# Kernel tuning notes

Hardware: AMD Instinct MI355X
Metric: run time of the kernel (lower is better)

## Reference

```python
import jax, jax.numpy as jnp
import numpy as np

EPS = 1e-5

def layer_norm(x, g, b):
    mu = jnp.mean(x, axis=-1, keepdims=True)
    var = jnp.var(x, axis=-1, keepdims=True)
    return (x - mu) * jax.lax.rsqrt(var + EPS) * g + b

def setup_inputs() -> dict:
    key = jax.random.key(0)
    ks = jax.random.split(key, 8)
    B, N, C, H = 4, 1024, 1024, 16
    Dh = C * 4
    std = 0.02
    return {
        "x": jax.random.normal(ks[0], (B, N, C), dtype=jnp.float32),
        "qkv_w": jax.random.normal(ks[1], (3 * C, C), dtype=jnp.float32) * std,
        "proj_w": jax.random.normal(ks[2], (C, C), dtype=jnp.float32) * std,
        "proj_b": jnp.zeros((C,), dtype=jnp.float32),
        "fc1_w": jax.random.normal(ks[3], (Dh, C), dtype=jnp.float32) * std,
        "fc1_b": jnp.zeros((Dh,), dtype=jnp.float32),
        "fc2_w": jax.random.normal(ks[4], (C, Dh), dtype=jnp.float32) * std,
        "fc2_b": jnp.zeros((C,), dtype=jnp.float32),
        "ln1_g": jnp.ones((C,), dtype=jnp.float32),
        "ln1_b": jnp.zeros((C,), dtype=jnp.float32),
        "ln2_g": jnp.ones((C,), dtype=jnp.float32),
        "ln2_b": jnp.zeros((C,), dtype=jnp.float32),
        "lnh_g": jnp.ones((Dh,), dtype=jnp.float32),
        "lnh_b": jnp.zeros((Dh,), dtype=jnp.float32),
    }

def reference(x, qkv_w, proj_w, proj_b, fc1_w, fc1_b, fc2_w, fc2_b,
              ln1_g, ln1_b, ln2_g, ln2_b, lnh_g, lnh_b):
    B, N, C = x.shape
    H = 16
    Dh = C // H
    scale = Dh ** (-0.5)

    # --- attention sublayer (pre-norm) ---
    h = layer_norm(x, ln1_g, ln1_b)
    qkv = (h @ qkv_w.T).reshape(B, N, 3, H, Dh).transpose(2, 0, 3, 1, 4)  # [3,B,H,N,Dh]
    q, k, v = qkv[0], qkv[1], qkv[2]
    attn = jnp.einsum('bhid,bhjd->bhij', q, k) * scale
    attn = jax.nn.softmax(attn, axis=-1)
    o = jnp.einsum('bhij,bhjd->bhid', attn, v)          # [B,H,N,Dh]
    o = o.transpose(0, 2, 1, 3).reshape(B, N, C)
    o = o @ proj_w.T + proj_b
    x = x + o

    # --- MLP sublayer (pre-norm, with LN on hidden per use_ln=True) ---
    h = layer_norm(x, ln2_g, ln2_b)
    u = jax.nn.gelu(h @ fc1_w.T + fc1_b, approximate=False)  # torch nn.GELU = erf form
    u = layer_norm(u, lnh_g, lnh_b)
    m = u @ fc2_w.T + fc2_b
    return x + m
```

## Files before the change

kernel.cpp:

```cpp
#include <hip/hip_runtime.h>
#include <hip/hip_bf16.h>
#include <math.h>


#define TOKENS 4096
#define CDIM   1024
#define HEADS  16
#define DHEAD  64
#define HID    4096

typedef __attribute__((ext_vector_type(4))) float  floatx4;
typedef __attribute__((ext_vector_type(8))) short  short8;

__device__ __forceinline__ void gl_lds16(const void* g, void* l)
{
    __builtin_amdgcn_global_load_lds(
        (const __attribute__((address_space(1))) unsigned int*)g,
        (__attribute__((address_space(3))) unsigned int*)l,
        16, 0, 0);
}

__global__ __launch_bounds__(256) void cvt_all(
    const float* __restrict__ s0, const float* __restrict__ s1,
    const float* __restrict__ s2, const float* __restrict__ s3,
    __hip_bfloat16* __restrict__ dst)
{
    long i = (long)blockIdx.x * 256 + threadIdx.x;
    const float* src;
    long base;
    if (i < 768l * 1024)       { src = s0; base = 0; }
    else if (i < 1792l * 1024) { src = s1; base = 768l * 1024; }
    else if (i < 2816l * 1024) { src = s2; base = 1792l * 1024; }
    else                       { src = s3; base = 2816l * 1024; }
    float4 v = ((const float4*)src)[i - base];
    __hip_bfloat16 t[4];
    t[0] = __float2bfloat16(v.x);
    t[1] = __float2bfloat16(v.y);
    t[2] = __float2bfloat16(v.z);
    t[3] = __float2bfloat16(v.w);
    *(uint2*)(dst + 4l * i) = *(uint2*)t;
}

__global__ __launch_bounds__(256) void ln_f32_kernel(
    const float* __restrict__ x, const float* __restrict__ g,
    const float* __restrict__ b, __hip_bfloat16* __restrict__ y, int C)
{
    int row = blockIdx.x;
    const float4* xr = (const float4*)(x + (long)row * C);
    uint2* yr = (uint2*)(y + (long)row * C);
    const int C4 = C >> 2;

    float s = 0.f, ss = 0.f;
    for (int i = threadIdx.x; i < C4; i += 256) {
        float4 v = xr[i];
        s  += v.x + v.y + v.z + v.w;
        ss += v.x * v.x + v.y * v.y + v.z * v.z + v.w * v.w;
    }
    #pragma unroll
    for (int d = 32; d; d >>= 1) {
        s  += __shfl_down(s, d);
        ss += __shfl_down(ss, d);
    }
    __shared__ float buf[4][2];
    int wid = threadIdx.x >> 6, lane = threadIdx.x & 63;
    if (lane == 0) { buf[wid][0] = s; buf[wid][1] = ss; }
    __syncthreads();
    if (threadIdx.x == 0) {
        s = buf[0][0] + buf[1][0] + buf[2][0] + buf[3][0];
        ss = buf[0][1] + buf[1][1] + buf[2][1] + buf[3][1];
        buf[0][0] = s; buf[0][1] = ss;
    }
    __syncthreads();
    s = buf[0][0]; ss = buf[0][1];

    float invC = 1.f / (float)C;
    float mu = s * invC;
    float var = ss * invC - mu * mu;
    float inv = rsqrtf(var + 1e-5f);
    const float4* gg = (const float4*)g;
    const float4* bb = (const float4*)b;
    for (int i = threadIdx.x; i < C4; i += 256) {
        float4 v = xr[i], gv = gg[i], bv = bb[i];
        __hip_bfloat16 t[4];
        t[0] = __float2bfloat16((v.x - mu) * inv * gv.x + bv.x);
        t[1] = __float2bfloat16((v.y - mu) * inv * gv.y + bv.y);
        t[2] = __float2bfloat16((v.z - mu) * inv * gv.z + bv.z);
        t[3] = __float2bfloat16((v.w - mu) * inv * gv.w + bv.w);
        yr[i] = *(uint2*)t;
    }
}

__global__ __launch_bounds__(256) void ln_bf16_kernel(
    const __hip_bfloat16* __restrict__ x, const float* __restrict__ g,
    const float* __restrict__ b, __hip_bfloat16* __restrict__ y, int C)
{
    int row = blockIdx.x;
    const uint4* xr = (const uint4*)(x + (long)row * C);
    uint4* yr = (uint4*)(y + (long)row * C);
    const int C8 = C >> 3;

    float s = 0.f, ss = 0.f;
    for (int i = threadIdx.x; i < C8; i += 256) {
        uint4 raw = xr[i];
        const __hip_bfloat16* p = (const __hip_bfloat16*)&raw;
        #pragma unroll
        for (int j = 0; j < 8; ++j) {
            float v = __bfloat162float(p[j]);
            s += v; ss += v * v;
        }
    }
    #pragma unroll
    for (int d = 32; d; d >>= 1) {
        s  += __shfl_down(s, d);
        ss += __shfl_down(ss, d);
    }
    __shared__ float buf[4][2];
    int wid = threadIdx.x >> 6, lane = threadIdx.x & 63;
    if (lane == 0) { buf[wid][0] = s; buf[wid][1] = ss; }
    __syncthreads();
    if (threadIdx.x == 0) {
        s = buf[0][0] + buf[1][0] + buf[2][0] + buf[3][0];
        ss = buf[0][1] + buf[1][1] + buf[2][1] + buf[3][1];
        buf[0][0] = s; buf[0][1] = ss;
    }
    __syncthreads();
    s = buf[0][0]; ss = buf[0][1];

    float invC = 1.f / (float)C;
    float mu = s * invC;
    float var = ss * invC - mu * mu;
    float inv = rsqrtf(var + 1e-5f);
    const float4* gg = (const float4*)g;
    const float4* bb = (const float4*)b;
    for (int i = threadIdx.x; i < C8; i += 256) {
        uint4 raw = xr[i];
        const __hip_bfloat16* p = (const __hip_bfloat16*)&raw;
        float4 g0 = gg[2 * i], g1 = gg[2 * i + 1];
        float4 b0 = bb[2 * i], b1 = bb[2 * i + 1];
        __hip_bfloat16 t[8];
        t[0] = __float2bfloat16((__bfloat162float(p[0]) - mu) * inv * g0.x + b0.x);
        t[1] = __float2bfloat16((__bfloat162float(p[1]) - mu) * inv * g0.y + b0.y);
        t[2] = __float2bfloat16((__bfloat162float(p[2]) - mu) * inv * g0.z + b0.z);
        t[3] = __float2bfloat16((__bfloat162float(p[3]) - mu) * inv * g0.w + b0.w);
        t[4] = __float2bfloat16((__bfloat162float(p[4]) - mu) * inv * g1.x + b1.x);
        t[5] = __float2bfloat16((__bfloat162float(p[5]) - mu) * inv * g1.y + b1.y);
        t[6] = __float2bfloat16((__bfloat162float(p[6]) - mu) * inv * g1.z + b1.z);
        t[7] = __float2bfloat16((__bfloat162float(p[7]) - mu) * inv * g1.w + b1.w);
        yr[i] = *(uint4*)t;
    }
}

__global__ __launch_bounds__(256, 2) void gemm_db(
    const __hip_bfloat16* __restrict__ A,
    const __hip_bfloat16* __restrict__ W,
    const float* __restrict__ bias, const float* __restrict__ residual,
    void* __restrict__ Cout, int M, int N, int K, int mode)
{
    __shared__ __align__(16) char Asl[2][16384];
    __shared__ __align__(16) char Bsl[2][16384];

    int tid = threadIdx.x;
    int wave = tid >> 6, lane = tid & 63;

    int mt, nt;
    {
        int gx = gridDim.x, gy = gridDim.y;
        int lin = blockIdx.y * gx + blockIdx.x;
        int chunk = gy >> 3;
        int xcd = lin & 7, q = lin >> 3;
        mt = xcd * chunk + (q % chunk);
        nt = q / chunk;
    }
    int bm = mt * 128, bn = nt * 128;
    int wm = wave & 1, wn = wave >> 1;
    int fm = lane & 15, quad = lane >> 4;
    const int r7 = fm & 7;

    const int nk = K / 64;

    const int rsub = lane >> 3;
    const int csub = (lane & 7) ^ rsub;
    const __hip_bfloat16* gA[4];
    const __hip_bfloat16* gB[4];
    int dseg[4];
    #pragma unroll
    for (int j = 0; j < 4; ++j) {
        int seg = wave * 4 + j;
        gA[j] = A + (long)(bm + seg * 8 + rsub) * K + csub * 8;
        gB[j] = W + (long)(bn + seg * 8 + rsub) * K + csub * 8;
        dseg[j] = seg * 1024;
    }

#define STAGE(b, kt) { \
    const long ko = (long)(kt) * 64; \
    _Pragma("unroll") \
    for (int j = 0; j < 4; ++j) { \
        gl_lds16(gA[j] + ko, Asl[b] + dseg[j]); \
        gl_lds16(gB[j] + ko, Bsl[b] + dseg[j]); \
    } }

    floatx4 acc[4][4] = {};

    STAGE(0, 0);
    __syncthreads();

    int cur = 0;
    for (int kt = 0; kt < nk; ++kt) {
        if (kt + 1 < nk) STAGE(cur ^ 1, kt + 1);

        const char* Ab = Asl[cur];
        const char* Bb = Bsl[cur];
        #pragma unroll
        for (int kh = 0; kh < 2; ++kh) {
            const int xsw = ((kh * 4 + quad) ^ r7) << 4;
            short8 bq[4];
            #pragma unroll
            for (int j = 0; j < 4; ++j)
                bq[j] = *(const short8*)(Bb + (wn * 64 + j * 16 + fm) * 128 + xsw);
            #pragma unroll
            for (int i = 0; i < 4; ++i) {
                short8 af = *(const short8*)(Ab + (wm * 64 + i * 16 + fm) * 128 + xsw);
                #pragma unroll
                for (int j = 0; j < 4; ++j)
                    acc[i][j] = __builtin_amdgcn_mfma_f32_16x16x32_bf16(
                        af, bq[j], acc[i][j], 0, 0, 0);
            }
        }
        __syncthreads();
        cur ^= 1;
    }
#undef STAGE

    int mbase = bm + wm * 64;
    int nbase = bn + wn * 64;
    if (mode == 2) {
        float* Cf = (float*)Cout;
        #pragma unroll
        for (int i = 0; i < 4; ++i) {
            #pragma unroll
            for (int j = 0; j < 4; ++j) {
                int ncol = nbase + j * 16 + fm;
                float bv = bias[ncol];
                #pragma unroll
                for (int r = 0; r < 4; ++r) {
                    int mrow = mbase + i * 16 + quad * 4 + r;
                    long idx = (long)mrow * N + ncol;
                    Cf[idx] = acc[i][j][r] + bv + residual[idx];
                }
            }
        }
    } else {
        __hip_bfloat16* Cb = (__hip_bfloat16*)Cout;
        #pragma unroll
        for (int i = 0; i < 4; ++i) {
            #pragma unroll
            for (int j = 0; j < 4; ++j) {
                int ncol = nbase + j * 16 + fm;
                #pragma unroll
                for (int r = 0; r < 4; ++r) {
                    int mrow = mbase + i * 16 + quad * 4 + r;
                    float v = acc[i][j][r];
                    if (bias) v += bias[ncol];
                    if (mode == 1) {
                        float z = v * (1.5957691216f + 0.0713548162f * v * v);
                        v = v / (1.f + __expf(-z));
                    }
                    Cb[(long)mrow * N + ncol] = __float2bfloat16(v);
                }
            }
        }
    }
}

__global__ __launch_bounds__(256) void attn_mfma(
    const __hip_bfloat16* __restrict__ qkv, __hip_bfloat16* __restrict__ o_out)
{
    __shared__ __align__(16) char Ks[2][64 * 144];
    __shared__ __align__(16) char Vt[2][64 * 144];
    __shared__ __align__(16) char Ps[4 * 16 * 144];

    const int C3 = 3 * CDIM;
    int lin = blockIdx.x;
    int xcd = lin & 7, q = lin >> 3;
    int bh = xcd * 8 + (q >> 4);
    int qt = q & 15;
    int b = bh >> 4, hh = bh & 15;
    int tid = threadIdx.x, wave = tid >> 6, lane = tid & 63;
    int l = lane & 15, quad = lane >> 4;

    const __hip_bfloat16* qrow =
        qkv + (long)(b * 1024 + qt * 64 + wave * 16 + l) * C3 + hh * DHEAD;
    short8 qf0 = *(const short8*)(qrow + quad * 8);
    short8 qf1 = *(const short8*)(qrow + 32 + quad * 8);

    char* Psw = Ps + wave * (16 * 144);

    int sc = tid & 7;
    int skl = tid >> 3;

    const __hip_bfloat16* Kbase = qkv + (long)(b * 1024) * C3 + CDIM + hh * DHEAD;
    const __hip_bfloat16* Vbase = qkv + (long)(b * 1024) * C3 + 2 * CDIM + hh * DHEAD;
    const int kpp = skl ^ (sc << 2);

    floatx4 facc[4] = {};
    float mrun = -1e30f, lrun = 0.f;

    uint4 kA0, kA1, vA0, vA1;
    uint4 kB0, kB1, vB0, vB1;

#define GKV(t, k0, k1, v0, v1) { \
    const __hip_bfloat16* Kg = Kbase + (long)((t) * 64) * C3; \
    const __hip_bfloat16* Vg = Vbase + (long)((t) * 64) * C3; \
    k0 = *(const uint4*)(Kg + (long)skl * C3 + sc * 8); \
    k1 = *(const uint4*)(Kg + (long)(skl + 32) * C3 + sc * 8); \
    v0 = *(const uint4*)(Vg + (long)(2 * skl) * C3 + sc * 8); \
    v1 = *(const uint4*)(Vg + (long)(2 * skl + 1) * C3 + sc * 8); }
#define WKV(bf, k0, k1, v0, v1) { \
    *(uint4*)(Ks[bf] + skl * 144 + sc * 16) = k0; \
    *(uint4*)(Ks[bf] + (skl + 32) * 144 + sc * 16) = k1; \
    const ushort* e0 = (const ushort*)&v0; \
    const ushort* e1 = (const ushort*)&v1; \
    _Pragma("unroll") \
    for (int j = 0; j < 8; ++j) { \
        unsigned dw = (unsigned)e0[j] | ((unsigned)e1[j] << 16); \
        *(unsigned*)(Vt[bf] + (sc * 8 + j) * 144 + kpp * 4) = dw; \
    } }

    auto compute = [&](int buf) {
        floatx4 st[4] = {};
        #pragma unroll
        for (int kb = 0; kb < 4; ++kb) {
            short8 k0 = *(const short8*)(Ks[buf] + (kb * 16 + l) * 144 + quad * 16);
            short8 k1 = *(const short8*)(Ks[buf] + (kb * 16 + l) * 144 + 64 + quad * 16);
            st[kb] = __builtin_amdgcn_mfma_f32_16x16x32_bf16(k0, qf0, st[kb], 0, 0, 0);
            st[kb] = __builtin_amdgcn_mfma_f32_16x16x32_bf16(k1, qf1, st[kb], 0, 0, 0);
        }
        float p[16];
        float tm = -1e30f;
        #pragma unroll
        for (int kb = 0; kb < 4; ++kb)
            #pragma unroll
            for (int r = 0; r < 4; ++r) {
                float s = st[kb][r] * 0.125f;
                p[kb * 4 + r] = s;
                tm = fmaxf(tm, s);
            }
        tm = fmaxf(tm, __shfl_xor(tm, 16));
        tm = fmaxf(tm, __shfl_xor(tm, 32));
        float mn = fmaxf(mrun, tm);
        float alpha = __expf(mrun - mn);
        float psum = 0.f;
        #pragma unroll
        for (int i = 0; i < 16; ++i) { p[i] = __expf(p[i] - mn); psum += p[i]; }
        psum += __shfl_xor(psum, 16);
        psum += __shfl_xor(psum, 32);
        lrun = lrun * alpha + psum;
        mrun = mn;

        #pragma unroll
        for (int kb = 0; kb < 4; ++kb) {
            __hip_bfloat16 t[4];
            #pragma unroll
            for (int r = 0; r < 4; ++r) t[r] = __float2bfloat16(p[kb * 4 + r]);
            *(uint2*)(Psw + l * 144 + kb * 32 + quad * 8) = *(const uint2*)t;
        }

        float a0 = __shfl(alpha, quad * 4 + 0);
        float a1 = __shfl(alpha, quad * 4 + 1);
        float a2 = __shfl(alpha, quad * 4 + 2);
        float a3 = __shfl(alpha, quad * 4 + 3);
        #pragma unroll
        for (int db = 0; db < 4; ++db) {
            facc[db][0] *= a0; facc[db][1] *= a1;
            facc[db][2] *= a2; facc[db][3] *= a3;
        }

        short8 pf0 = *(const short8*)(Psw + l * 144 + quad * 16);
        short8 pf1 = *(const short8*)(Psw + l * 144 + 64 + quad * 16);
        #pragma unroll
        for (int db = 0; db < 4; ++db) {
            int d = db * 16 + l;
            int o3 = (d >> 3) & 7;
            short8 v0 = *(const short8*)(Vt[buf] + d * 144 + ((quad ^ o3) << 4));
            short8 v1 = *(const short8*)(Vt[buf] + d * 144 + (((4 + quad) ^ o3) << 4));
            facc[db] = __builtin_amdgcn_mfma_f32_16x16x32_bf16(pf0, v0, facc[db], 0, 0, 0);
            facc[db] = __builtin_amdgcn_mfma_f32_16x16x32_bf16(pf1, v1, facc[db], 0, 0, 0);
        }
    };

    GKV(0, kA0, kA1, vA0, vA1);
    #pragma unroll 1
    for (int kt = 0; kt < 16; kt += 2) {
        WKV(0, kA0, kA1, vA0, vA1);
        __syncthreads();
        GKV(kt + 1, kB0, kB1, vB0, vB1);
        compute(0);
        WKV(1, kB0, kB1, vB0, vB1);
        __syncthreads();
        if (kt + 2 < 16) GKV(kt + 2, kA0, kA1, vA0, vA1);
        compute(1);
    }
#undef GKV
#undef WKV

    float il0 = 1.f / __shfl(lrun, quad * 4 + 0);
    float il1 = 1.f / __shfl(lrun, quad * 4 + 1);
    float il2 = 1.f / __shfl(lrun, quad * 4 + 2);
    float il3 = 1.f / __shfl(lrun, quad * 4 + 3);
    __hip_bfloat16* orow =
        o_out + (long)(b * 1024 + qt * 64 + wave * 16) * CDIM + hh * DHEAD;
    #pragma unroll
    for (int db = 0; db < 4; ++db) {
        int col = db * 16 + l;
        orow[(quad * 4 + 0) * CDIM + col] = __float2bfloat16(facc[db][0] * il0);
        orow[(quad * 4 + 1) * CDIM + col] = __float2bfloat16(facc[db][1] * il1);
        orow[(quad * 4 + 2) * CDIM + col] = __float2bfloat16(facc[db][2] * il2);
        orow[(quad * 4 + 3) * CDIM + col] = __float2bfloat16(facc[db][3] * il3);
    }
}

extern "C" void kernel_launch(void* const* d_in, const int* in_sizes, int n_in,
                              void* d_out, int out_size, void* d_ws, size_t ws_size,
                              hipStream_t stream)
{
    const float* x      = (const float*)d_in[0];
    const float* qkv_w  = (const float*)d_in[1];
    const float* proj_w = (const float*)d_in[2];
    const float* proj_b = (const float*)d_in[3];
    const float* fc1_w  = (const float*)d_in[4];
    const float* fc1_b  = (const float*)d_in[5];
    const float* fc2_w  = (const float*)d_in[6];
    const float* fc2_b  = (const float*)d_in[7];
    const float* ln1_g  = (const float*)d_in[8];
    const float* ln1_b  = (const float*)d_in[9];
    const float* ln2_g  = (const float*)d_in[10];
    const float* ln2_b  = (const float*)d_in[11];
    const float* lnh_g  = (const float*)d_in[12];
    const float* lnh_b  = (const float*)d_in[13];

    float* out = (float*)d_out;

    __hip_bfloat16* wsb     = (__hip_bfloat16*)d_ws;
    __hip_bfloat16* qkvw_bf = wsb;
    __hip_bfloat16* fc1w_bf = qkvw_bf + 3l * 1024 * 1024;
    __hip_bfloat16* fc2w_bf = fc1w_bf + 4l * 1024 * 1024;
    __hip_bfloat16* projw_bf= fc2w_bf + 4l * 1024 * 1024;
    __hip_bfloat16* h_bf    = projw_bf + 1l * 1024 * 1024;
    __hip_bfloat16* qkv_bf  = h_bf + 4l * 1024 * 1024;
    __hip_bfloat16* o_bf    = qkv_bf + 12l * 1024 * 1024;
    __hip_bfloat16* u_bf    = o_bf + 4l * 1024 * 1024;

    cvt_all<<<12288, 256, 0, stream>>>(qkv_w, fc1_w, fc2_w, proj_w, qkvw_bf);

    ln_f32_kernel<<<TOKENS, 256, 0, stream>>>(x, ln1_g, ln1_b, h_bf, CDIM);
    gemm_db<<<dim3(3072 / 128, TOKENS / 128), 256, 0, stream>>>(
        h_bf, qkvw_bf, nullptr, nullptr, qkv_bf, TOKENS, 3072, CDIM, 0);
    attn_mfma<<<1024, 256, 0, stream>>>(qkv_bf, o_bf);
    gemm_db<<<dim3(CDIM / 128, TOKENS / 128), 256, 0, stream>>>(
        o_bf, projw_bf, proj_b, x, out, TOKENS, CDIM, CDIM, 2);
    ln_f32_kernel<<<TOKENS, 256, 0, stream>>>(out, ln2_g, ln2_b, h_bf, CDIM);
    gemm_db<<<dim3(HID / 128, TOKENS / 128), 256, 0, stream>>>(
        h_bf, fc1w_bf, fc1_b, nullptr, u_bf, TOKENS, HID, CDIM, 1);
    ln_bf16_kernel<<<TOKENS, 256, 0, stream>>>(u_bf, lnh_g, lnh_b, u_bf, HID);
    gemm_db<<<dim3(CDIM / 128, TOKENS / 128), 256, 0, stream>>>(
        u_bf, fc2w_bf, fc2_b, out, out, TOKENS, CDIM, HID, 2);
}
```

Measured before the change: 386.7 us.

## Split GEMM into K=32 128x128 kernel and 64x64 tile kernel for N=1024 GEMMs

Replaces the single 128x128, K=64 double-buffered GEMM with two specialized kernels. For the wide QKV and FC1 GEMMs, a 128x128 tile with K-step 32 halves LDS usage, which allows 4 blocks per CU and uses a new swizzled layout packing two 64-row halves per LDS row. For the narrow proj and FC2 GEMMs (N=1024), a 64x64 tile kernel launches 4x more blocks to fill the GPU, but each block gets less data reuse and runs more k-iteration syncs.

```diff
diff --git a/kernel.cpp b/kernel.cpp
--- a/kernel.cpp
+++ b/kernel.cpp
@@ -150,14 +150,14 @@
     }
 }
 
-__global__ __launch_bounds__(256, 2) void gemm_db(
+__global__ __launch_bounds__(256, 4) void gemm32q(
     const __hip_bfloat16* __restrict__ A,
     const __hip_bfloat16* __restrict__ W,
-    const float* __restrict__ bias, const float* __restrict__ residual,
-    void* __restrict__ Cout, int M, int N, int K, int mode)
-{
-    __shared__ __align__(16) char Asl[2][16384];
-    __shared__ __align__(16) char Bsl[2][16384];
+    const float* __restrict__ bias,
+    __hip_bfloat16* __restrict__ Cout, int M, int N, int K, int mode)
+{
+    __shared__ __align__(16) char Asl[2][8192];
+    __shared__ __align__(16) char Bsl[2][8192];
 
     int tid = threadIdx.x;
     int wave = tid >> 6, lane = tid & 63;
@@ -174,32 +174,137 @@
     int bm = mt * 128, bn = nt * 128;
     int wm = wave & 1, wn = wave >> 1;
     int fm = lane & 15, quad = lane >> 4;
-    const int r7 = fm & 7;
+
+    const int nk = K / 32;
+
+    const int rsub  = lane >> 3;
+    const int cphys = lane & 7;
+    const int clog  = cphys ^ rsub;
+    const __hip_bfloat16* gA[2];
+    const __hip_bfloat16* gB[2];
+    int dseg[2];
+    #pragma unroll
+    for (int j = 0; j < 2; ++j) {
+        int seg = wave * 2 + j;
+        int ldsrow = seg * 8 + rsub;
+        int mrow = ldsrow + 64 * (clog >> 2);
+        int koff = (clog & 3) * 8;
+        gA[j] = A + (long)(bm + mrow) * K + koff;
+        gB[j] = W + (long)(bn + mrow) * K + koff;
+        dseg[j] = seg * 1024;
+    }
+
+#define STAGE(b, kt) { \
+    const long ko = (long)(kt) * 32; \
+    _Pragma("unroll") \
+    for (int j = 0; j < 2; ++j) { \
+        gl_lds16(gA[j] + ko, Asl[b] + dseg[j]); \
+        gl_lds16(gB[j] + ko, Bsl[b] + dseg[j]); \
+    } }
+
+    floatx4 acc[4][4] = {};
+
+    STAGE(0, 0);
+    __syncthreads();
+
+    const int xswA = (((wm * 4 + quad) ^ (fm & 7)) << 4);
+    const int xswB = (((wn * 4 + quad) ^ (fm & 7)) << 4);
+
+    int cur = 0;
+    for (int kt = 0; kt < nk; ++kt) {
+        if (kt + 1 < nk) STAGE(cur ^ 1, kt + 1);
+
+        const char* Ab = Asl[cur];
+        const char* Bb = Bsl[cur];
+        short8 bq[4];
+        #pragma unroll
+        for (int j = 0; j < 4; ++j)
+            bq[j] = *(const short8*)(Bb + (j * 16 + fm) * 128 + xswB);
+        #pragma unroll
+        for (int i = 0; i < 4; ++i) {
+            short8 af = *(const short8*)(Ab + (i * 16 + fm) * 128 + xswA);
+            #pragma unroll
+            for (int j = 0; j < 4; ++j)
+                acc[i][j] = __builtin_amdgcn_mfma_f32_16x16x32_bf16(
+                    af, bq[j], acc[i][j], 0, 0, 0);
+        }
+        __syncthreads();
+        cur ^= 1;
+    }
+#undef STAGE
+
+    int mbase = bm + wm * 64;
+    int nbase = bn + wn * 64;
+    #pragma unroll
+    for (int i = 0; i < 4; ++i) {
+        #pragma unroll
+        for (int j = 0; j < 4; ++j) {
+            int ncol = nbase + j * 16 + fm;
+            #pragma unroll
+            for (int r = 0; r < 4; ++r) {
+                int mrow = mbase + i * 16 + quad * 4 + r;
+                float v = acc[i][j][r];
+                if (bias) v += bias[ncol];
+                if (mode == 1) {
+                    float z = v * (1.5957691216f + 0.0713548162f * v * v);
+                    v = v / (1.f + __expf(-z));
+                }
+                Cout[(long)mrow * N + ncol] = __float2bfloat16(v);
+            }
+        }
+    }
+}
+
+__global__ __launch_bounds__(256, 4) void gemm64g(
+    const __hip_bfloat16* __restrict__ A,
+    const __hip_bfloat16* __restrict__ W,
+    const float* __restrict__ bias, const float* __restrict__ residual,
+    float* __restrict__ Cout, int M, int N, int K)
+{
+    __shared__ __align__(16) char Asl[2][8192];
+    __shared__ __align__(16) char Bsl[2][8192];
+
+    int tid = threadIdx.x;
+    int wave = tid >> 6, lane = tid & 63;
+
+    int mt, nt;
+    {
+        int gx = gridDim.x, gy = gridDim.y;
+        int lin = blockIdx.y * gx + blockIdx.x;
+        int chunk = gy >> 3;
+        int xcd = lin & 7, q = lin >> 3;
+        mt = xcd * chunk + (q % chunk);
+        nt = q / chunk;
+    }
+    int bm = mt * 64, bn = nt * 64;
+    int wm = wave & 1, wn = wave >> 1;
+    int fm = lane & 15, quad = lane >> 4;
 
     const int nk = K / 64;
 
     const int rsub = lane >> 3;
-    const int csub = (lane & 7) ^ rsub;
-    const __hip_bfloat16* gA[4];
-    const __hip_bfloat16* gB[4];
-    int dseg[4];
-    #pragma unroll
-    for (int j = 0; j < 4; ++j) {
-        int seg = wave * 4 + j;
-        gA[j] = A + (long)(bm + seg * 8 + rsub) * K + csub * 8;
-        gB[j] = W + (long)(bn + seg * 8 + rsub) * K + csub * 8;
+    const int csrc = (lane & 7) ^ rsub;
+    const __hip_bfloat16* gA[2];
+    const __hip_bfloat16* gB[2];
+    int dseg[2];
+    #pragma unroll
+    for (int j = 0; j < 2; ++j) {
+        int seg = wave * 2 + j;
+        int row = seg * 8 + rsub;
+        gA[j] = A + (long)(bm + row) * K + csrc * 8;
+        gB[j] = W + (long)(bn + row) * K + csrc * 8;
         dseg[j] = seg * 1024;
     }
 
 #define STAGE(b, kt) { \
     const long ko = (long)(kt) * 64; \
     _Pragma("unroll") \
-    for (int j = 0; j < 4; ++j) { \
+    for (int j = 0; j < 2; ++j) { \
         gl_lds16(gA[j] + ko, Asl[b] + dseg[j]); \
         gl_lds16(gB[j] + ko, Bsl[b] + dseg[j]); \
     } }
 
-    floatx4 acc[4][4] = {};
+    floatx4 acc[2][2] = {};
 
     STAGE(0, 0);
     __syncthreads();
@@ -212,61 +317,34 @@
         const char* Bb = Bsl[cur];
         #pragma unroll
         for (int kh = 0; kh < 2; ++kh) {
-            const int xsw = ((kh * 4 + quad) ^ r7) << 4;
-            short8 bq[4];
-            #pragma unroll
-            for (int j = 0; j < 4; ++j)
-                bq[j] = *(const short8*)(Bb + (wn * 64 + j * 16 + fm) * 128 + xsw);
-            #pragma unroll
-            for (int i = 0; i < 4; ++i) {
-                short8 af = *(const short8*)(Ab + (wm * 64 + i * 16 + fm) * 128 + xsw);
-                #pragma unroll
-                for (int j = 0; j < 4; ++j)
-                    acc[i][j] = __builtin_amdgcn_mfma_f32_16x16x32_bf16(
-                        af, bq[j], acc[i][j], 0, 0, 0);
-            }
+            const int xsw = (((kh * 4 + quad) ^ (fm & 7)) << 4);
+            short8 b0 = *(const short8*)(Bb + (wn * 32 + fm) * 128 + xsw);
+            short8 b1 = *(const short8*)(Bb + (wn * 32 + 16 + fm) * 128 + xsw);
+            short8 a0 = *(const short8*)(Ab + (wm * 32 + fm) * 128 + xsw);
+            short8 a1 = *(const short8*)(Ab + (wm * 32 + 16 + fm) * 128 + xsw);
+            acc[0][0] = __builtin_amdgcn_mfma_f32_16x16x32_bf16(a0, b0, acc[0][0], 0, 0, 0);
+            acc[0][1] = __builtin_amdgcn_mfma_f32_16x16x32_bf16(a0, b1, acc[0][1], 0, 0, 0);
+            acc[1][0] = __builtin_amdgcn_mfma_f32_16x16x32_bf16(a1, b0, acc[1][0], 0, 0, 0);
+            acc[1][1] = __builtin_amdgcn_mfma_f32_16x16x32_bf16(a1, b1, acc[1][1], 0, 0, 0);
         }
         __syncthreads();
         cur ^= 1;
     }
 #undef STAGE
 
-    int mbase = bm + wm * 64;
-    int nbase = bn + wn * 64;
-    if (mode == 2) {
-        float* Cf = (float*)Cout;
-        #pragma unroll
-        for (int i = 0; i < 4; ++i) {
+    int mbase = bm + wm * 32;
+    int nbase = bn + wn * 32;
+    #pragma unroll
+    for (int i = 0; i < 2; ++i) {
+        #pragma unroll
+        for (int j = 0; j < 2; ++j) {
+            int ncol = nbase + j * 16 + fm;
+            float bv = bias[ncol];
             #pragma unroll
-            for (int j = 0; j < 4; ++j) {
-                int ncol = nbase + j * 16 + fm;
-                float bv = bias[ncol];
-                #pragma unroll
-                for (int r = 0; r < 4; ++r) {
-                    int mrow = mbase + i * 16 + quad * 4 + r;
-                    long idx = (long)mrow * N + ncol;
-                    Cf[idx] = acc[i][j][r] + bv + residual[idx];
-                }
-            }
-        }
-    } else {
-        __hip_bfloat16* Cb = (__hip_bfloat16*)Cout;
-        #pragma unroll
-        for (int i = 0; i < 4; ++i) {
-            #pragma unroll
-            for (int j = 0; j < 4; ++j) {
-                int ncol = nbase + j * 16 + fm;
-                #pragma unroll
-                for (int r = 0; r < 4; ++r) {
-                    int mrow = mbase + i * 16 + quad * 4 + r;
-                    float v = acc[i][j][r];
-                    if (bias) v += bias[ncol];
-                    if (mode == 1) {
-                        float z = v * (1.5957691216f + 0.0713548162f * v * v);
-                        v = v / (1.f + __expf(-z));
-                    }
-                    Cb[(long)mrow * N + ncol] = __float2bfloat16(v);
-                }
+            for (int r = 0; r < 4; ++r) {
+                int mrow = mbase + i * 16 + quad * 4 + r;
+                long idx = (long)mrow * N + ncol;
+                Cout[idx] = acc[i][j][r] + bv + residual[idx];
             }
         }
     }
@@ -453,15 +531,15 @@
     cvt_all<<<12288, 256, 0, stream>>>(qkv_w, fc1_w, fc2_w, proj_w, qkvw_bf);
 
     ln_f32_kernel<<<TOKENS, 256, 0, stream>>>(x, ln1_g, ln1_b, h_bf, CDIM);
-    gemm_db<<<dim3(3072 / 128, TOKENS / 128), 256, 0, stream>>>(
-        h_bf, qkvw_bf, nullptr, nullptr, qkv_bf, TOKENS, 3072, CDIM, 0);
+    gemm32q<<<dim3(3072 / 128, TOKENS / 128), 256, 0, stream>>>(
+        h_bf, qkvw_bf, nullptr, qkv_bf, TOKENS, 3072, CDIM, 0);
     attn_mfma<<<1024, 256, 0, stream>>>(qkv_bf, o_bf);
-    gemm_db<<<dim3(CDIM / 128, TOKENS / 128), 256, 0, stream>>>(
-        o_bf, projw_bf, proj_b, x, out, TOKENS, CDIM, CDIM, 2);
+    gemm64g<<<dim3(CDIM / 64, TOKENS / 64), 256, 0, stream>>>(
+        o_bf, projw_bf, proj_b, x, out, TOKENS, CDIM, CDIM);
     ln_f32_kernel<<<TOKENS, 256, 0, stream>>>(out, ln2_g, ln2_b, h_bf, CDIM);
-    gemm_db<<<dim3(HID / 128, TOKENS / 128), 256, 0, stream>>>(
-        h_bf, fc1w_bf, fc1_b, nullptr, u_bf, TOKENS, HID, CDIM, 1);
+    gemm32q<<<dim3(HID / 128, TOKENS / 128), 256, 0, stream>>>(
+        h_bf, fc1w_bf, fc1_b, u_bf, TOKENS, HID, CDIM, 1);
     ln_bf16_kernel<<<TOKENS, 256, 0, stream>>>(u_bf, lnh_g, lnh_b, u_bf, HID);
-    gemm_db<<<dim3(CDIM / 128, TOKENS / 128), 256, 0, stream>>>(
-        u_bf, fc2w_bf, fc2_b, out, out, TOKENS, CDIM, HID, 2);
-}
+    gemm64g<<<dim3(CDIM / 64, TOKENS / 64), 256, 0, stream>>>(
+        u_bf, fc2w_bf, fc2_b, out, out, TOKENS, CDIM, HID);
+}
```

New measurement: 347.6 us (median of 2 runs). 10.1% less time.
